# Performance work log

Measured on AMD Instinct MI355X. Metric: run time of the kernel, lower is better.

## Reference

```python
import jax, jax.numpy as jnp
import numpy as np

N_HEADS = 16


def setup_inputs() -> dict:
    key = jax.random.key(0)
    ks = jax.random.split(key, 8)
    B, S, D = 4, 2048, 1024
    scale = 1.0 / np.sqrt(D)
    return {
        "x": jax.random.normal(ks[0], (B, S, D), dtype=jnp.float32),
        "Wq": jax.random.normal(ks[1], (D, D), dtype=jnp.float32) * scale,
        "bq": jax.random.normal(ks[2], (D,), dtype=jnp.float32) * 0.01,
        "Wk": jax.random.normal(ks[3], (D, D), dtype=jnp.float32) * scale,
        "bk": jax.random.normal(ks[4], (D,), dtype=jnp.float32) * 0.01,
        "Wv": jax.random.normal(ks[5], (D, D), dtype=jnp.float32) * scale,
        "bv": jax.random.normal(ks[6], (D,), dtype=jnp.float32) * 0.01,
        "mask": jax.random.randint(ks[7], (B, S), 0, 2, dtype=jnp.int32),
    }


def reference(x, Wq, bq, Wk, bk, Wv, bv, mask):
    B, S, D = x.shape
    H = N_HEADS
    W = D // H
    # QKV projections (Linear with weight stored input-major: y = x @ W + b)
    q = (x @ Wq + bq).reshape(B, S, H, W).transpose(0, 2, 1, 3)  # (B,H,S,W)
    k = (x @ Wk + bk).reshape(B, S, H, W).transpose(0, 2, 1, 3)
    v = (x @ Wv + bv).reshape(B, S, H, W).transpose(0, 2, 1, 3)
    # scaled dot-product scores: (B,H,S,S)
    scores = jnp.einsum("bhsw,bhtw->bhst", q, k) / jnp.sqrt(jnp.asarray(W, x.dtype))
    # mask==1 means masked (subtract large constant), per original code
    scores = scores - 10000.0 * mask[:, None, None, :].astype(x.dtype)
    attn = jax.nn.softmax(scores, axis=-1)  # dropout p=0 -> identity
    h = jnp.einsum("bhst,bhtw->bhsw", attn, v)  # (B,H,S,W)
    h = h.transpose(0, 2, 1, 3).reshape(B, S, D)
    return h
```

## Files before the change

### kernel.cpp

```cpp
#include <hip/hip_runtime.h>
#include <math.h>

#define B_NUM 4
#define S_LEN 2048
#define D_DIM 1024
#define H_NUM 16
#define W_DIM 64

typedef float4 f4;
typedef _Float16 f16;
typedef f16 f16x8 __attribute__((ext_vector_type(8)));
typedef f16 f16x4 __attribute__((ext_vector_type(4)));
typedef float floatx4 __attribute__((ext_vector_type(4)));

#define GLOAD_LDS16(gp, lp)                                                     \
    __builtin_amdgcn_global_load_lds(                                           \
        (const __attribute__((address_space(1))) void*)(gp),                    \
        (__attribute__((address_space(3))) void*)(lp), 16, 0, 0)

__global__ __launch_bounds__(256) void compact_kernel(
    const int* __restrict__ mask, short* __restrict__ invmap,
    int* __restrict__ cnt)
{
    __shared__ int sc[256];
    const int b   = blockIdx.x;
    const int tid = threadIdx.x;
    const int t0  = tid * 8;

    int kept[8], c = 0;
#pragma unroll
    for (int j = 0; j < 8; ++j) {
        kept[j] = (mask[b * S_LEN + t0 + j] == 0);
        c += kept[j];
    }
    sc[tid] = c;
    __syncthreads();
    for (int off = 1; off < 256; off <<= 1) {
        int add = (tid >= off) ? sc[tid - off] : 0;
        __syncthreads();
        sc[tid] += add;
        __syncthreads();
    }
    int base = sc[tid] - c;
#pragma unroll
    for (int j = 0; j < 8; ++j) {
        invmap[b * S_LEN + t0 + j] = kept[j] ? (short)(base++) : (short)-1;
    }
    if (tid == 255) {
        cnt[b * 2 + 0] = sc[255];
        cnt[b * 2 + 1] = (sc[255] + 63) & ~63;
    }
}

__global__ __launch_bounds__(256) void cast_x_kernel(
    const float* __restrict__ x, f16* __restrict__ x16)
{
    const size_t i = (size_t)blockIdx.x * 256 + threadIdx.x;
    f4 t = *(const f4*)&x[i * 4];
    f16x4 o;
    o[0] = (f16)t.x; o[1] = (f16)t.y; o[2] = (f16)t.z; o[3] = (f16)t.w;
    *(f16x4*)&x16[i * 4] = o;
}

__global__ __launch_bounds__(256) void transpose_w_kernel(
    const float* __restrict__ Wq, const float* __restrict__ Wk,
    const float* __restrict__ Wv, f16* __restrict__ wt16)
{
    __shared__ float ts[64][68];

    const int tid = threadIdx.x;
    const int k0 = blockIdx.x * 64;
    const int n0 = blockIdx.y * 64;
    const float* Wsel = (blockIdx.z == 0) ? Wq : (blockIdx.z == 1) ? Wk : Wv;
    f16* outp = wt16 + (size_t)blockIdx.z * D_DIM * D_DIM;

    const int r  = tid >> 4;
    const int c4 = (tid & 15) * 4;
#pragma unroll
    for (int i = 0; i < 4; ++i) {
        f4 t = *(const f4*)&Wsel[(size_t)(k0 + r + i * 16) * D_DIM + n0 + c4];
        *(f4*)&ts[r + i * 16][c4] = t;
    }
    __syncthreads();
#pragma unroll
    for (int i = 0; i < 4; ++i) {
        int idx = tid + i * 256;
        int nl = idx >> 4;
        int k4 = (idx & 15) * 4;
        f16x4 o;
#pragma unroll
        for (int j = 0; j < 4; ++j) o[j] = (f16)ts[k4 + j][nl];
        *(f16x4*)&outp[(size_t)(n0 + nl) * D_DIM + k0 + k4] = o;
    }
}

__global__ __launch_bounds__(256) void qkv_mfma_kernel(
    const f16* __restrict__ x16, const f16* __restrict__ wt16,
    const float* __restrict__ bq, const float* __restrict__ bk,
    const float* __restrict__ bv, const short* __restrict__ invmap,
    f16* __restrict__ Qo, f16* __restrict__ Ko, f16* __restrict__ Vo)
{
    __shared__ f16 As[128 * 64];
    __shared__ f16 Bs[128 * 64];

    const int tid  = threadIdx.x;
    const int lane = tid & 63;
    const int wid  = tid >> 6;
    const int lx   = lane & 15;
    const int quad = lane >> 4;
    const int wm   = wid >> 1;
    const int wn   = wid & 1;

    const int r0   = blockIdx.y * 128;
    const int nt   = blockIdx.x;
    const int midx = nt >> 3;
    const int c0   = (nt & 7) * 128;

    const f16* Ag = x16 + (size_t)r0 * D_DIM;
    const f16* Bg = wt16 + (size_t)midx * D_DIM * D_DIM + (size_t)c0 * D_DIM;

    const int srow = lane >> 3;
    const int scol = (lane & 7) * 8;

    floatx4 acc[4][4];
#pragma unroll
    for (int a = 0; a < 4; ++a)
#pragma unroll
        for (int b = 0; b < 4; ++b) { acc[a][b][0]=0.f; acc[a][b][1]=0.f; acc[a][b][2]=0.f; acc[a][b][3]=0.f; }

    for (int k0 = 0; k0 < D_DIM; k0 += 64) {
        __syncthreads();
#pragma unroll
        for (int it = 0; it < 4; ++it) {
            int chunk = wid * 4 + it;
            int row   = chunk * 8 + srow;
            GLOAD_LDS16(&Ag[(size_t)row * D_DIM + k0 + scol], &As[chunk * 512]);
            GLOAD_LDS16(&Bg[(size_t)row * D_DIM + k0 + scol], &Bs[chunk * 512]);
        }
        __syncthreads();

#pragma unroll
        for (int kh = 0; kh < 2; ++kh) {
            f16x8 af[4], bf[4];
#pragma unroll
            for (int tm = 0; tm < 4; ++tm)
                af[tm] = *(const f16x8*)&As[(wm * 64 + tm * 16 + lx) * 64 + kh * 32 + quad * 8];
#pragma unroll
            for (int tn = 0; tn < 4; ++tn)
                bf[tn] = *(const f16x8*)&Bs[(wn * 64 + tn * 16 + lx) * 64 + kh * 32 + quad * 8];
#pragma unroll
            for (int tm = 0; tm < 4; ++tm)
#pragma unroll
                for (int tn = 0; tn < 4; ++tn)
                    acc[tm][tn] = __builtin_amdgcn_mfma_f32_16x16x32_f16(
                        af[tm], bf[tn], acc[tm][tn], 0, 0, 0);
        }
    }

    const float* bp = (midx == 0) ? bq : (midx == 1) ? bk : bv;
    float bias[4];
#pragma unroll
    for (int tn = 0; tn < 4; ++tn)
        bias[tn] = bp[c0 + wn * 64 + tn * 16 + lx];

    if (midx == 0) {
#pragma unroll
        for (int tm = 0; tm < 4; ++tm) {
            int grb = r0 + wm * 64 + tm * 16 + quad * 4;
            int b = grb >> 11, s = grb & (S_LEN - 1);
#pragma unroll
            for (int tn = 0; tn < 4; ++tn) {
                int gc = c0 + wn * 64 + tn * 16 + lx;
                int h = gc >> 6, w = gc & 63;
                size_t base = (((size_t)(b * H_NUM + h)) * S_LEN + s) * W_DIM + w;
#pragma unroll
                for (int rr = 0; rr < 4; ++rr)
                    Qo[base + (size_t)rr * W_DIM] =
                        (f16)((acc[tm][tn][rr] + bias[tn]) * 0.125f);
            }
        }
    } else if (midx == 1) {
#pragma unroll
        for (int tm = 0; tm < 4; ++tm) {
            int grb = r0 + wm * 64 + tm * 16 + quad * 4;
            int b = grb >> 11, s = grb & (S_LEN - 1);
            short jc[4];
#pragma unroll
            for (int rr = 0; rr < 4; ++rr) jc[rr] = invmap[b * S_LEN + s + rr];
#pragma unroll
            for (int tn = 0; tn < 4; ++tn) {
                int gc = c0 + wn * 64 + tn * 16 + lx;
                int h = gc >> 6, w = gc & 63;
#pragma unroll
                for (int rr = 0; rr < 4; ++rr)
                    if (jc[rr] >= 0)
                        Ko[(((size_t)(b * H_NUM + h)) * S_LEN + jc[rr]) * W_DIM + w] =
                            (f16)(acc[tm][tn][rr] + bias[tn]);
            }
        }
    } else {
#pragma unroll
        for (int tm = 0; tm < 4; ++tm) {
            int grb = r0 + wm * 64 + tm * 16 + quad * 4;
            int b = grb >> 11, s = grb & (S_LEN - 1);
            short jc[4];
#pragma unroll
            for (int rr = 0; rr < 4; ++rr) jc[rr] = invmap[b * S_LEN + s + rr];
#pragma unroll
            for (int tn = 0; tn < 4; ++tn) {
                int gc = c0 + wn * 64 + tn * 16 + lx;
                int h = gc >> 6, w = gc & 63;
#pragma unroll
                for (int rr = 0; rr < 4; ++rr)
                    if (jc[rr] >= 0)
                        Vo[(((size_t)(b * H_NUM + h)) * W_DIM + w) * S_LEN + jc[rr]] =
                            (f16)(acc[tm][tn][rr] + bias[tn]);
            }
        }
    }
}

#define LSTR 72

__global__ __launch_bounds__(256) void attn_kernel(
    const f16* __restrict__ Q, const f16* __restrict__ Kc,
    const f16* __restrict__ Vct, const int* __restrict__ cnt,
    float* __restrict__ out)
{
    __shared__ f16 Ks[64][LSTR];
    __shared__ f16 Vs[64][LSTR];

    const int tid  = threadIdx.x;
    const int lane = tid & 63;
    const int wid  = tid >> 6;
    const int lx   = lane & 15;
    const int quad = lane >> 4;
    const int qt = blockIdx.x, h = blockIdx.y, bb = blockIdx.z;

    const int count = cnt[bb * 2 + 0];
    const int scp   = cnt[bb * 2 + 1];

    const size_t hoff = ((size_t)(bb * H_NUM + h)) * S_LEN * W_DIM;
    const f16* Qg = Q + hoff + (size_t)qt * 128 * W_DIM;
    const f16* Kg = Kc + hoff;
    const f16* Vg = Vct + hoff;

    f16x8 qb[2][2];
#pragma unroll
    for (int u = 0; u < 2; ++u) {
        int qrow = u * 64 + wid * 16 + lx;
        qb[u][0] = *(const f16x8*)&Qg[(size_t)qrow * W_DIM + quad * 8];
        qb[u][1] = *(const f16x8*)&Qg[(size_t)qrow * W_DIM + 32 + quad * 8];
    }

    floatx4 o[2][4];
    float lsum[2] = {0.f, 0.f};
#pragma unroll
    for (int u = 0; u < 2; ++u)
#pragma unroll
        for (int wb = 0; wb < 4; ++wb) { o[u][wb][0]=0.f; o[u][wb][1]=0.f; o[u][wb][2]=0.f; o[u][wb][3]=0.f; }

    for (int k0 = 0; k0 < scp; k0 += 64) {
        __syncthreads();
#pragma unroll
        for (int it = 0; it < 2; ++it) {
            int idx = tid + it * 256;
            int row = idx >> 3, c8 = (idx & 7) * 8;
            *(f16x8*)&Ks[row][c8] = *(const f16x8*)&Kg[(size_t)(k0 + row) * W_DIM + c8];
            *(f16x8*)&Vs[row][c8] = *(const f16x8*)&Vg[(size_t)row * S_LEN + k0 + c8];
        }
        __syncthreads();

        const bool tail = (k0 + 64 > count);

        f16x4 pb[2][4];
#pragma unroll
        for (int n = 0; n < 4; ++n) {
            f16x8 ka0 = *(const f16x8*)&Ks[n * 16 + lx][quad * 8];
            f16x8 ka1 = *(const f16x8*)&Ks[n * 16 + lx][32 + quad * 8];
            const int kb = k0 + n * 16 + quad * 4;
#pragma unroll
            for (int u = 0; u < 2; ++u) {
                floatx4 s; s[0]=0.f; s[1]=0.f; s[2]=0.f; s[3]=0.f;
                s = __builtin_amdgcn_mfma_f32_16x16x32_f16(ka0, qb[u][0], s, 0, 0, 0);
                s = __builtin_amdgcn_mfma_f32_16x16x32_f16(ka1, qb[u][1], s, 0, 0, 0);
                float p[4], ls = 0.f;
                if (tail) {
#pragma unroll
                    for (int r = 0; r < 4; ++r) {
                        float sv = (kb + r < count) ? s[r] : -1.0e4f;
                        p[r] = __expf(sv); ls += p[r];
                    }
                } else {
#pragma unroll
                    for (int r = 0; r < 4; ++r) { p[r] = __expf(s[r]); ls += p[r]; }
                }
                lsum[u] += ls;
#pragma unroll
                for (int r = 0; r < 4; ++r) pb[u][n][r] = (f16)p[r];
            }
        }

#pragma unroll
        for (int wb = 0; wb < 4; ++wb) {
#pragma unroll
            for (int n = 0; n < 4; ++n) {
                f16x4 va = *(const f16x4*)&Vs[wb * 16 + lx][n * 16 + quad * 4];
#pragma unroll
                for (int u = 0; u < 2; ++u)
                    o[u][wb] = __builtin_amdgcn_mfma_f32_16x16x16f16(va, pb[u][n], o[u][wb], 0, 0, 0);
            }
        }
    }

#pragma unroll
    for (int u = 0; u < 2; ++u) {
        float ls = lsum[u];
        ls += __shfl_xor(ls, 16);
        ls += __shfl_xor(ls, 32);
        const float rl = 1.0f / ls;
        const int q = qt * 128 + u * 64 + wid * 16 + lx;
        const size_t base = ((size_t)bb * S_LEN + q) * D_DIM + h * W_DIM;
#pragma unroll
        for (int wb = 0; wb < 4; ++wb) {
            f4 r;
            r.x = o[u][wb][0] * rl;
            r.y = o[u][wb][1] * rl;
            r.z = o[u][wb][2] * rl;
            r.w = o[u][wb][3] * rl;
            *(f4*)&out[base + wb * 16 + quad * 4] = r;
        }
    }
}

extern "C" void kernel_launch(void* const* d_in, const int* in_sizes, int n_in,
                              void* d_out, int out_size, void* d_ws, size_t ws_size,
                              hipStream_t stream)
{
    const float* x    = (const float*)d_in[0];
    const float* Wq   = (const float*)d_in[1];
    const float* bq   = (const float*)d_in[2];
    const float* Wk   = (const float*)d_in[3];
    const float* bk   = (const float*)d_in[4];
    const float* Wv   = (const float*)d_in[5];
    const float* bv   = (const float*)d_in[6];
    const int*   mask = (const int*)d_in[7];
    float* out = (float*)d_out;

    const size_t per = (size_t)B_NUM * H_NUM * S_LEN * W_DIM;
    f16*   Q      = (f16*)d_ws;
    f16*   Kc     = Q + per;
    f16*   Vct    = Kc + per;
    f16*   x16    = Vct + per;
    f16*   wt16   = x16 + (size_t)(B_NUM * S_LEN) * D_DIM;
    int*   cnt    = (int*)(wt16 + (size_t)3 * D_DIM * D_DIM);
    short* invmap = (short*)(cnt + 2 * B_NUM);

    compact_kernel<<<B_NUM, 256, 0, stream>>>(mask, invmap, cnt);
    cast_x_kernel<<<(B_NUM * S_LEN * D_DIM) / 1024, 256, 0, stream>>>(x, x16);
    transpose_w_kernel<<<dim3(16, 16, 3), 256, 0, stream>>>(Wq, Wk, Wv, wt16);
    qkv_mfma_kernel<<<dim3(24, 64), 256, 0, stream>>>(
        x16, wt16, bq, bk, bv, invmap, Q, Kc, Vct);
    attn_kernel<<<dim3(S_LEN / 128, H_NUM, B_NUM), 256, 0, stream>>>(
        Q, Kc, Vct, cnt, out);
}
```

Baseline: 244.5 us.

## Gather kept rows for K/V projection and skip fully masked row tiles

The compaction kernel now writes a forward map from compacted index to source row, replacing the inverse map. The QKV GEMM uses it to gather only unmasked rows of x for the K and V projections, and blocks beyond the padded kept count exit early, so about half the K/V GEMM work is skipped. K and V stores become contiguous, with V written as vectorized f16x4, and LDS tiles use an XOR swizzle to cut bank conflicts. Padded rows past the kept count gather row 0 (the map is zero-filled), which is safe only if attention ignores indices at or beyond count. Zero-filling the map and storing a third count add a small cost in the compaction kernel.

```diff
diff --git a/kernel.cpp b/kernel.cpp
--- a/kernel.cpp
+++ b/kernel.cpp
@@ -19,7 +19,7 @@
         (__attribute__((address_space(3))) void*)(lp), 16, 0, 0)
 
 __global__ __launch_bounds__(256) void compact_kernel(
-    const int* __restrict__ mask, short* __restrict__ invmap,
+    const int* __restrict__ mask, short* __restrict__ fwdmap,
     int* __restrict__ cnt)
 {
     __shared__ int sc[256];
@@ -27,6 +27,9 @@
     const int tid = threadIdx.x;
     const int t0  = tid * 8;
 
+#pragma unroll
+    for (int j = 0; j < 8; ++j) fwdmap[b * S_LEN + t0 + j] = 0;
+
     int kept[8], c = 0;
 #pragma unroll
     for (int j = 0; j < 8; ++j) {
@@ -43,12 +46,12 @@
     }
     int base = sc[tid] - c;
 #pragma unroll
-    for (int j = 0; j < 8; ++j) {
-        invmap[b * S_LEN + t0 + j] = kept[j] ? (short)(base++) : (short)-1;
-    }
+    for (int j = 0; j < 8; ++j)
+        if (kept[j]) fwdmap[b * S_LEN + (base++)] = (short)(t0 + j);
     if (tid == 255) {
-        cnt[b * 2 + 0] = sc[255];
-        cnt[b * 2 + 1] = (sc[255] + 63) & ~63;
+        cnt[b * 4 + 0] = sc[255];
+        cnt[b * 4 + 1] = (sc[255] + 63) & ~63;
+        cnt[b * 4 + 2] = (sc[255] + 127) & ~127;
     }
 }
 
@@ -97,7 +100,8 @@
 __global__ __launch_bounds__(256) void qkv_mfma_kernel(
     const f16* __restrict__ x16, const f16* __restrict__ wt16,
     const float* __restrict__ bq, const float* __restrict__ bk,
-    const float* __restrict__ bv, const short* __restrict__ invmap,
+    const float* __restrict__ bv, const short* __restrict__ fwdmap,
+    const int* __restrict__ cnt,
     f16* __restrict__ Qo, f16* __restrict__ Ko, f16* __restrict__ Vo)
 {
     __shared__ f16 As[128 * 64];
@@ -111,16 +115,28 @@
     const int wm   = wid >> 1;
     const int wn   = wid & 1;
 
-    const int r0   = blockIdx.y * 128;
-    const int nt   = blockIdx.x;
-    const int midx = nt >> 3;
-    const int c0   = (nt & 7) * 128;
-
-    const f16* Ag = x16 + (size_t)r0 * D_DIM;
+    const int r0    = blockIdx.y * 128;
+    const int nt    = blockIdx.x;
+    const int midx  = nt >> 3;
+    const int c0    = (nt & 7) * 128;
+    const int bB    = r0 >> 11;
+    const int r0loc = r0 & (S_LEN - 1);
+
+    if (midx > 0 && r0loc >= cnt[bB * 4 + 2]) return;
+
     const f16* Bg = wt16 + (size_t)midx * D_DIM * D_DIM + (size_t)c0 * D_DIM;
 
     const int srow = lane >> 3;
-    const int scol = (lane & 7) * 8;
+    const int scw  = ((lane & 7) ^ srow) * 8;
+
+    int arows[4];
+#pragma unroll
+    for (int it = 0; it < 4; ++it) {
+        int rl = (wid * 4 + it) * 8 + srow;
+        arows[it] = (midx == 0)
+            ? (r0 + rl)
+            : (bB * S_LEN + (int)fwdmap[bB * S_LEN + r0loc + rl]);
+    }
 
     floatx4 acc[4][4];
 #pragma unroll
@@ -133,21 +149,21 @@
 #pragma unroll
         for (int it = 0; it < 4; ++it) {
             int chunk = wid * 4 + it;
-            int row   = chunk * 8 + srow;
-            GLOAD_LDS16(&Ag[(size_t)row * D_DIM + k0 + scol], &As[chunk * 512]);
-            GLOAD_LDS16(&Bg[(size_t)row * D_DIM + k0 + scol], &Bs[chunk * 512]);
+            GLOAD_LDS16(&x16[(size_t)arows[it] * D_DIM + k0 + scw], &As[chunk * 512]);
+            GLOAD_LDS16(&Bg[(size_t)(chunk * 8 + srow) * D_DIM + k0 + scw], &Bs[chunk * 512]);
         }
         __syncthreads();
 
 #pragma unroll
         for (int kh = 0; kh < 2; ++kh) {
+            const int csw = ((kh * 4 + quad) ^ (lx & 7)) * 8;
             f16x8 af[4], bf[4];
 #pragma unroll
             for (int tm = 0; tm < 4; ++tm)
-                af[tm] = *(const f16x8*)&As[(wm * 64 + tm * 16 + lx) * 64 + kh * 32 + quad * 8];
+                af[tm] = *(const f16x8*)&As[(wm * 64 + tm * 16 + lx) * 64 + csw];
 #pragma unroll
             for (int tn = 0; tn < 4; ++tn)
-                bf[tn] = *(const f16x8*)&Bs[(wn * 64 + tn * 16 + lx) * 64 + kh * 32 + quad * 8];
+                bf[tn] = *(const f16x8*)&Bs[(wn * 64 + tn * 16 + lx) * 64 + csw];
 #pragma unroll
             for (int tm = 0; tm < 4; ++tm)
 #pragma unroll
@@ -166,13 +182,12 @@
     if (midx == 0) {
 #pragma unroll
         for (int tm = 0; tm < 4; ++tm) {
-            int grb = r0 + wm * 64 + tm * 16 + quad * 4;
-            int b = grb >> 11, s = grb & (S_LEN - 1);
+            int s = r0loc + wm * 64 + tm * 16 + quad * 4;
 #pragma unroll
             for (int tn = 0; tn < 4; ++tn) {
                 int gc = c0 + wn * 64 + tn * 16 + lx;
                 int h = gc >> 6, w = gc & 63;
-                size_t base = (((size_t)(b * H_NUM + h)) * S_LEN + s) * W_DIM + w;
+                size_t base = (((size_t)(bB * H_NUM + h)) * S_LEN + s) * W_DIM + w;
 #pragma unroll
                 for (int rr = 0; rr < 4; ++rr)
                     Qo[base + (size_t)rr * W_DIM] =
@@ -182,39 +197,29 @@
     } else if (midx == 1) {
 #pragma unroll
         for (int tm = 0; tm < 4; ++tm) {
-            int grb = r0 + wm * 64 + tm * 16 + quad * 4;
-            int b = grb >> 11, s = grb & (S_LEN - 1);
-            short jc[4];
-#pragma unroll
-            for (int rr = 0; rr < 4; ++rr) jc[rr] = invmap[b * S_LEN + s + rr];
+            int jc = r0loc + wm * 64 + tm * 16 + quad * 4;
 #pragma unroll
             for (int tn = 0; tn < 4; ++tn) {
                 int gc = c0 + wn * 64 + tn * 16 + lx;
                 int h = gc >> 6, w = gc & 63;
+                size_t base = (((size_t)(bB * H_NUM + h)) * S_LEN + jc) * W_DIM + w;
 #pragma unroll
                 for (int rr = 0; rr < 4; ++rr)
-                    if (jc[rr] >= 0)
-                        Ko[(((size_t)(b * H_NUM + h)) * S_LEN + jc[rr]) * W_DIM + w] =
-                            (f16)(acc[tm][tn][rr] + bias[tn]);
+                    Ko[base + (size_t)rr * W_DIM] = (f16)(acc[tm][tn][rr] + bias[tn]);
             }
         }
     } else {
 #pragma unroll
         for (int tm = 0; tm < 4; ++tm) {
-            int grb = r0 + wm * 64 + tm * 16 + quad * 4;
-            int b = grb >> 11, s = grb & (S_LEN - 1);
-            short jc[4];
-#pragma unroll
-            for (int rr = 0; rr < 4; ++rr) jc[rr] = invmap[b * S_LEN + s + rr];
+            int jc = r0loc + wm * 64 + tm * 16 + quad * 4;
 #pragma unroll
             for (int tn = 0; tn < 4; ++tn) {
                 int gc = c0 + wn * 64 + tn * 16 + lx;
                 int h = gc >> 6, w = gc & 63;
-#pragma unroll
-                for (int rr = 0; rr < 4; ++rr)
-                    if (jc[rr] >= 0)
-                        Vo[(((size_t)(b * H_NUM + h)) * W_DIM + w) * S_LEN + jc[rr]] =
-                            (f16)(acc[tm][tn][rr] + bias[tn]);
+                f16x4 v;
+#pragma unroll
+                for (int rr = 0; rr < 4; ++rr) v[rr] = (f16)(acc[tm][tn][rr] + bias[tn]);
+                *(f16x4*)&Vo[(((size_t)(bB * H_NUM + h)) * W_DIM + w) * S_LEN + jc] = v;
             }
         }
     }
@@ -237,8 +242,8 @@
     const int quad = lane >> 4;
     const int qt = blockIdx.x, h = blockIdx.y, bb = blockIdx.z;
 
-    const int count = cnt[bb * 2 + 0];
-    const int scp   = cnt[bb * 2 + 1];
+    const int count = cnt[bb * 4 + 0];
+    const int scp   = cnt[bb * 4 + 1];
 
     const size_t hoff = ((size_t)(bb * H_NUM + h)) * S_LEN * W_DIM;
     const f16* Qg = Q + hoff + (size_t)qt * 128 * W_DIM;
@@ -354,13 +359,13 @@
     f16*   x16    = Vct + per;
     f16*   wt16   = x16 + (size_t)(B_NUM * S_LEN) * D_DIM;
     int*   cnt    = (int*)(wt16 + (size_t)3 * D_DIM * D_DIM);
-    short* invmap = (short*)(cnt + 2 * B_NUM);
-
-    compact_kernel<<<B_NUM, 256, 0, stream>>>(mask, invmap, cnt);
+    short* fwdmap = (short*)(cnt + 4 * B_NUM);
+
+    compact_kernel<<<B_NUM, 256, 0, stream>>>(mask, fwdmap, cnt);
     cast_x_kernel<<<(B_NUM * S_LEN * D_DIM) / 1024, 256, 0, stream>>>(x, x16);
     transpose_w_kernel<<<dim3(16, 16, 3), 256, 0, stream>>>(Wq, Wk, Wv, wt16);
     qkv_mfma_kernel<<<dim3(24, 64), 256, 0, stream>>>(
-        x16, wt16, bq, bk, bv, invmap, Q, Kc, Vct);
+        x16, wt16, bq, bk, bv, fwdmap, cnt, Q, Kc, Vct);
     attn_kernel<<<dim3(S_LEN / 128, H_NUM, B_NUM), 256, 0, stream>>>(
         Q, Kc, Vct, cnt, out);
 }
```

New measurement: 222.2 us. 1.1x faster.
